# Kernel optimization log

Measured on AMD Instinct MI355X. Metric: run time of the kernel, lower is better.

The kernel has to match this reference:

```python
import jax, jax.numpy as jnp
import numpy as np

# Config (matches init_kwargs): channels=64, num_ell=16 (lmax=3), correlation=3,
# num_elements=10, output irreps L=0 (dim 1) and L=1 (dim 3), n_nodes=2048.
N, C, I, E = 2048, 64, 16, 10
K3, K2, K1 = 4, 2, 1  # number of coupling paths per correlation order
DIMS = (1, 3)         # output irrep dims (0e, 1o)


def setup_inputs() -> dict:
    key = jax.random.key(0)
    ks = jax.random.split(key, 24)
    inp = {}
    inp['node_feats'] = jax.random.normal(ks[0], (N, C, I), dtype=jnp.float32)
    inp['sc'] = jax.random.normal(ks[1], (N, sum(C * d for d in DIMS)), dtype=jnp.float32)
    idx = jax.random.randint(ks[2], (N,), 0, E)
    inp['node_attrs'] = jax.nn.one_hot(idx, E, dtype=jnp.float32)
    # Clebsch-Gordan-structured basis tensors (random placeholders, correct shapes)
    for t, d in enumerate(DIMS):
        inp[f'U3_{t}'] = 0.1 * jax.random.normal(ks[3 + 6 * t], (d, I, I, I, K3), dtype=jnp.float32)
        inp[f'U2_{t}'] = 0.1 * jax.random.normal(ks[4 + 6 * t], (d, I, I, K2), dtype=jnp.float32)
        inp[f'U1_{t}'] = 0.1 * jax.random.normal(ks[5 + 6 * t], (d, I, K1), dtype=jnp.float32)
        inp[f'W3_{t}'] = jax.random.normal(ks[6 + 6 * t], (E, K3, C), dtype=jnp.float32) / np.sqrt(K3)
        inp[f'W2_{t}'] = jax.random.normal(ks[7 + 6 * t], (E, K2, C), dtype=jnp.float32) / np.sqrt(K2)
        inp[f'W1_{t}'] = jax.random.normal(ks[8 + 6 * t], (E, K1, C), dtype=jnp.float32)
        inp[f'Wlin_{t}'] = jax.random.normal(ks[15 + t], (C, C), dtype=jnp.float32)
    return inp


def _contract_irrep(x, y, U3, U2, U1, W3, W2, W1):
    # MACE Contraction: highest correlation first, then fold in x one order at a time.
    out = jnp.einsum('mijlk,ekc,bcl,be->bcmij', U3, W3, x, y)   # [N,C,d,I,I]
    c2 = jnp.einsum('mijk,ekc,be->bcmij', U2, W2, y) + out
    out = jnp.einsum('bcmij,bcj->bcmi', c2, x)                   # [N,C,d,I]
    c1 = jnp.einsum('mik,ekc,be->bcmi', U1, W1, y) + out
    return jnp.einsum('bcmi,bci->bcm', c1, x)                    # [N,C,d]


def reference(node_feats, sc, node_attrs,
              U3_0, U2_0, U1_0, W3_0, W2_0, W1_0, Wlin_0,
              U3_1, U2_1, U1_1, W3_1, W2_1, W1_1, Wlin_1):
    x, y = node_feats, node_attrs
    f0 = _contract_irrep(x, y, U3_0, U2_0, U1_0, W3_0, W2_0, W1_0)  # [N,C,1]
    f1 = _contract_irrep(x, y, U3_1, U2_1, U1_1, W3_1, W2_1, W1_1)  # [N,C,3]
    inv_sqrt_c = 1.0 / np.sqrt(C).astype(np.float32)
    l0 = jnp.einsum('bcd,cf->bfd', f0, Wlin_0) * inv_sqrt_c
    l1 = jnp.einsum('bcd,cf->bfd', f1, Wlin_1) * inv_sqrt_c
    out = jnp.concatenate([l0.reshape(l0.shape[0], -1), l1.reshape(l1.shape[0], -1)], axis=1)
    return out + sc
```

## Files before the change

### kernel.cpp

```cpp
#include <hip/hip_runtime.h>

#define NND   2048
#define NC    64
#define NI    16
#define NE    10
#define NT3   816
#define NT2   136
#define NPAD  1024
#define CHUNK 32
#define MAXIT 74
#define M2ST  36

#define OFF_U3S   0u
#define OFF_U2S   52224u
#define OFF_TBL2  56576u
#define OFF_PTBL  60672u
#define OFF_NLIST 61248u
#define OFF_BST   69440u
#define OFF_ITEMS 69504u
#define OFF_NIT   69824u
#define OFF_F     69888u

__device__ inline void unrank3(int p, int& i, int& j, int& l) {
  int rem = p, i_ = 0;
  for (;;) { int cnt = (16 - i_) * (17 - i_) / 2; if (rem < cnt) break; rem -= cnt; ++i_; }
  int j_ = i_;
  for (;;) { int cnt = 16 - j_; if (rem < cnt) break; rem -= cnt; ++j_; }
  i = i_; j = j_; l = j_ + rem;
}
__device__ inline void unrank2(int q, int& i, int& j) {
  int rem = q, i_ = 0;
  for (;;) { int cnt = 16 - i_; if (rem < cnt) break; rem -= cnt; ++i_; }
  i = i_; j = i_ + rem;
}
__device__ inline int rank2(int a, int b) { return a * 16 - (a * (a - 1)) / 2 + (b - a); }

__device__ inline float4 u3read(const float* U3, int m, int a, int b, int d) {
  return *(const float4*)(U3 + (size_t)((((m * 16 + a) * 16 + b) * 16 + d) * 4));
}
__device__ inline float4 f4mul(float4 a, float4 b) {
  return make_float4(a.x * b.x, a.y * b.y, a.z * b.z, a.w * b.w);
}

__global__ __launch_bounds__(256) void k_prep(
    const float* __restrict__ U3_0, const float* __restrict__ U3_1,
    const float* __restrict__ U2_0, const float* __restrict__ U2_1,
    const float* __restrict__ y,
    float* __restrict__ U3sym, float* __restrict__ U2sym,
    int* __restrict__ tbl2, int* __restrict__ ptbl, int* __restrict__ nlist,
    int* __restrict__ bstart, int* __restrict__ items, int* __restrict__ nitems) {
  int tid = threadIdx.x;
  int bid = blockIdx.x;
  if (bid == 0) {
    for (int p = tid; p < NPAD; p += 256) {
      int a, qq;
      if (p < NT3) {
        int i, j, l; unrank3(p, i, j, l);
        a = l; qq = rank2(i, j);
      } else if (p < NT3 + NT2) {
        a = 16; qq = p - NT3;
      } else if (p < NT3 + NT2 + 16) {
        a = 16; qq = 136 + (p - NT3 - NT2);
      } else {
        a = 16; qq = 152;
      }
      tbl2[p] = a | (qq << 8);
    }
    for (int q = tid; q < NT2; q += 256) {
      int i, j; unrank2(q, i, j);
      ptbl[q] = i | (j << 8);
    }
    for (int idx = tid; idx < 4 * NT2; idx += 256) {
      int m4 = idx / NT2, q = idx - m4 * NT2;
      const float* U2 = (m4 == 0) ? U2_0 : U2_1;
      int mloc = (m4 == 0) ? 0 : (m4 - 1);
      int i, j; unrank2(q, i, j);
      const float* ua = U2 + (size_t)(((mloc * 16 + i) * 16 + j) * 2);
      float s0 = ua[0], s1 = ua[1];
      if (i != j) {
        const float* ub = U2 + (size_t)(((mloc * 16 + j) * 16 + i) * 2);
        s0 += ub[0]; s1 += ub[1];
      }
      float* o = U2sym + (size_t)(m4 * NT2 + q) * 2;
      o[0] = s0; o[1] = s1;
    }
  } else if (bid == 1) {
    __shared__ int cnt[NE], cur[NE];
    if (tid < NE) cnt[tid] = 0;
    __syncthreads();
    int mye[NND / 256];
    for (int rr = 0; rr < NND / 256; ++rr) {
      int b = tid + rr * 256;
      int e = 0;
      for (int ee = 0; ee < NE; ++ee)
        if (y[b * NE + ee] > 0.5f) e = ee;
      mye[rr] = e;
      atomicAdd(&cnt[e], 1);
    }
    __syncthreads();
    if (tid == 0) {
      int run = 0, ni = 0;
      for (int e = 0; e < NE; ++e) {
        bstart[e] = run; cur[e] = run;
        int nchunks = (cnt[e] + CHUNK - 1) / CHUNK;
        for (int ch = 0; ch < nchunks; ++ch) items[ni++] = e | (ch << 4);
        run += cnt[e];
      }
      bstart[NE] = run;
      nitems[0] = ni;
    }
    __syncthreads();
    for (int rr = 0; rr < NND / 256; ++rr) {
      int b = tid + rr * 256;
      int pos = atomicAdd(&cur[mye[rr]], 1);
      nlist[pos] = b;
    }
  } else {
    int idx = (bid - 2) * 256 + tid;
    if (idx < 4 * NT3) {
      int m4 = idx / NT3, tau = idx - m4 * NT3;
      const float* U3 = (m4 == 0) ? U3_0 : U3_1;
      int mloc = (m4 == 0) ? 0 : (m4 - 1);
      int i, j, l; unrank3(tau, i, j, l);
      float4 s = u3read(U3, mloc, i, j, l);
      if (i == j && j == l) {
      } else if (i == j) {
        float4 b1 = u3read(U3, mloc, i, l, i), b2 = u3read(U3, mloc, l, i, i);
        s.x += b1.x + b2.x; s.y += b1.y + b2.y; s.z += b1.z + b2.z; s.w += b1.w + b2.w;
      } else if (j == l) {
        float4 b1 = u3read(U3, mloc, j, i, j), b2 = u3read(U3, mloc, j, j, i);
        s.x += b1.x + b2.x; s.y += b1.y + b2.y; s.z += b1.z + b2.z; s.w += b1.w + b2.w;
      } else {
        float4 b1 = u3read(U3, mloc, i, l, j), b2 = u3read(U3, mloc, j, i, l);
        float4 b3 = u3read(U3, mloc, j, l, i), b4 = u3read(U3, mloc, l, i, j);
        float4 b5 = u3read(U3, mloc, l, j, i);
        s.x += b1.x + b2.x + b3.x + b4.x + b5.x;
        s.y += b1.y + b2.y + b3.y + b4.y + b5.y;
        s.z += b1.z + b2.z + b3.z + b4.z + b5.z;
        s.w += b1.w + b2.w + b3.w + b4.w + b5.w;
      }
      ((float4*)U3sym)[m4 * NT3 + tau] = s;
    }
  }
}

__device__ inline float4 mergef4(float4 x, float4 y, int m, int lane) {
  float4 r;
  bool hi = (lane & m) != 0;
  { float t = x.x + __shfl_xor(x.x, m); float u = y.x + __shfl_xor(y.x, m); r.x = hi ? u : t; }
  { float t = x.y + __shfl_xor(x.y, m); float u = y.y + __shfl_xor(y.y, m); r.y = hi ? u : t; }
  { float t = x.z + __shfl_xor(x.z, m); float u = y.z + __shfl_xor(y.z, m); r.z = hi ? u : t; }
  { float t = x.w + __shfl_xor(x.w, m); float u = y.w + __shfl_xor(y.w, m); r.w = hi ? u : t; }
  return r;
}

__global__ __launch_bounds__(256) void k_main(
    const float* __restrict__ x,
    const float* __restrict__ U3sym, const float* __restrict__ U2sym,
    const float* __restrict__ U1_0, const float* __restrict__ U1_1,
    const float* __restrict__ W3_0, const float* __restrict__ W3_1,
    const float* __restrict__ W2_0, const float* __restrict__ W2_1,
    const float* __restrict__ W1_0, const float* __restrict__ W1_1,
    const int* __restrict__ tbl2, const int* __restrict__ ptbl,
    const int* __restrict__ nlist, const int* __restrict__ bstart,
    const int* __restrict__ items, const int* __restrict__ nitems,
    float* __restrict__ f) {
  int bx = blockIdx.x;
  if (bx >= nitems[0]) return;
  __shared__ __align__(16) float4 sS4[NPAD];
  __shared__ __align__(16) float  sM2[153 * M2ST];
  __shared__ __align__(16) float  sxT[17 * M2ST];
  int tid = threadIdx.x;
  int w = tid >> 6, lane = tid & 63;
  int item = items[bx];
  int e = item & 15, ch = item >> 4;
  int c = blockIdx.y;
  int bs = bstart[e], be = bstart[e + 1];
  int base = bs + ch * CHUNK;
  int n_here = be - base; if (n_here > CHUNK) n_here = CHUNK;

  int t2r[16];
#pragma unroll
  for (int q = 0; q < 16; ++q) t2r[q] = tbl2[lane + (q << 6)];

  float w30[4], w31[4], w20[2], w21[2];
#pragma unroll
  for (int k = 0; k < 4; ++k) {
    w30[k] = W3_0[e * 256 + k * 64 + c];
    w31[k] = W3_1[e * 256 + k * 64 + c];
  }
#pragma unroll
  for (int k = 0; k < 2; ++k) {
    w20[k] = W2_0[e * 128 + k * 64 + c];
    w21[k] = W2_1[e * 128 + k * 64 + c];
  }
  float w10 = W1_0[e * 64 + c], w11 = W1_1[e * 64 + c];

  const float4* U3s4 = (const float4*)U3sym;
  float4 sreg[4];
#pragma unroll
  for (int k = 0; k < 4; ++k) {
    int p = tid + (k << 8);
    float4 o = make_float4(0.f, 0.f, 0.f, 0.f);
    if (p < NT3) {
      float4 u0 = U3s4[p];
      float4 u1 = U3s4[NT3 + p];
      float4 u2 = U3s4[2 * NT3 + p];
      float4 u3 = U3s4[3 * NT3 + p];
      o.x = u0.x * w30[0] + u0.y * w30[1] + u0.z * w30[2] + u0.w * w30[3];
      o.y = u1.x * w31[0] + u1.y * w31[1] + u1.z * w31[2] + u1.w * w31[3];
      o.z = u2.x * w31[0] + u2.y * w31[1] + u2.z * w31[2] + u2.w * w31[3];
      o.w = u3.x * w31[0] + u3.y * w31[1] + u3.z * w31[2] + u3.w * w31[3];
    } else if (p < NT3 + NT2) {
      int q = p - NT3;
      const float* u0 = U2sym + (size_t)(0 * NT2 + q) * 2;
      const float* u1 = U2sym + (size_t)(1 * NT2 + q) * 2;
      const float* u2 = U2sym + (size_t)(2 * NT2 + q) * 2;
      const float* u3 = U2sym + (size_t)(3 * NT2 + q) * 2;
      o.x = u0[0] * w20[0] + u0[1] * w20[1];
      o.y = u1[0] * w21[0] + u1[1] * w21[1];
      o.z = u2[0] * w21[0] + u2[1] * w21[1];
      o.w = u3[0] * w21[0] + u3[1] * w21[1];
    } else if (p < NT3 + NT2 + 16) {
      int i = p - NT3 - NT2;
      o.x = U1_0[i] * w10;
      o.y = U1_1[i] * w11;
      o.z = U1_1[16 + i] * w11;
      o.w = U1_1[32 + i] * w11;
    }
    sS4[p] = o;
    sreg[k] = o;
  }
  for (int rr = 0; rr < 2; ++rr) {
    int r = (tid >> 4) + 16 * rr, i = tid & 15;
    float v = 0.f;
    if (r < n_here) {
      int b = nlist[base + r];
      v = x[(size_t)b * (NC * NI) + c * NI + i];
    }
    sxT[i * M2ST + r] = v;
  }
  if (tid < CHUNK) sxT[16 * M2ST + tid] = 1.0f;
  __syncthreads();
  for (int idx = tid; idx < 153 * 8; idx += 256) {
    int qq = idx >> 3, rq = (idx & 7) << 2;
    float4 v;
    if (qq < NT2) {
      int pv = ptbl[qq];
      float4 xi = *(const float4*)&sxT[(pv & 255) * M2ST + rq];
      float4 xj = *(const float4*)&sxT[(pv >> 8) * M2ST + rq];
      v = f4mul(xi, xj);
    } else if (qq < 152) {
      v = *(const float4*)&sxT[(qq - 136) * M2ST + rq];
    } else {
      v = make_float4(0.f, 0.f, 0.f, 0.f);
    }
    *(float4*)&sM2[qq * M2ST + rq] = v;
  }
  __syncthreads();

  float4 acc[8];
#pragma unroll
  for (int t = 0; t < 8; ++t) acc[t] = make_float4(0.f, 0.f, 0.f, 0.f);
  int rbase = 8 * w;
#pragma unroll
  for (int q = 0; q < 16; ++q) {
    int t2 = t2r[q];
    int ai = t2 & 255, qq = t2 >> 8;
    float4 xa = *(const float4*)&sxT[ai * M2ST + rbase];
    float4 xb = *(const float4*)&sxT[ai * M2ST + rbase + 4];
    float4 ma = *(const float4*)&sM2[qq * M2ST + rbase];
    float4 mb = *(const float4*)&sM2[qq * M2ST + rbase + 4];
    float4 sv;
    if ((q & 3) == w) sv = sreg[q >> 2];
    else              sv = sS4[lane + (q << 6)];
    float mo[8];
    mo[0] = xa.x * ma.x; mo[1] = xa.y * ma.y; mo[2] = xa.z * ma.z; mo[3] = xa.w * ma.w;
    mo[4] = xb.x * mb.x; mo[5] = xb.y * mb.y; mo[6] = xb.z * mb.z; mo[7] = xb.w * mb.w;
#pragma unroll
    for (int t = 0; t < 8; ++t) {
      acc[t].x = fmaf(sv.x, mo[t], acc[t].x);
      acc[t].y = fmaf(sv.y, mo[t], acc[t].y);
      acc[t].z = fmaf(sv.z, mo[t], acc[t].z);
      acc[t].w = fmaf(sv.w, mo[t], acc[t].w);
    }
  }
  float4 s01 = mergef4(acc[0], acc[1], 32, lane);
  float4 s23 = mergef4(acc[2], acc[3], 32, lane);
  float4 s45 = mergef4(acc[4], acc[5], 32, lane);
  float4 s67 = mergef4(acc[6], acc[7], 32, lane);
  float4 t0 = mergef4(s01, s23, 16, lane);
  float4 t1 = mergef4(s45, s67, 16, lane);
  float4 u = mergef4(t0, t1, 8, lane);
#pragma unroll
  for (int m = 4; m >= 1; m >>= 1) {
    u.x += __shfl_xor(u.x, m);
    u.y += __shfl_xor(u.y, m);
    u.z += __shfl_xor(u.z, m);
    u.w += __shfl_xor(u.w, m);
  }
  if ((lane & 7) == 0) {
    int k = ((lane >> 5) & 1) | (((lane >> 4) & 1) << 1) | (((lane >> 3) & 1) << 2);
    int r = rbase + k;
    if (r < n_here) {
      float4* fo = (float4*)f;
      fo[(size_t)nlist[base + r] * 64 + c] = u;
    }
  }
}

__global__ __launch_bounds__(256) void k_out(
    const float* __restrict__ f, const float* __restrict__ Wl0,
    const float* __restrict__ Wl1, const float* __restrict__ sc,
    float* __restrict__ out) {
  __shared__ float sW0[4096], sW1[4096], sf[4][256];
  int tid = threadIdx.x;
  for (int u = tid; u < 4096; u += 256) { sW0[u] = Wl0[u]; sW1[u] = Wl1[u]; }
  int nb = blockIdx.x * 4;
  for (int u = tid; u < 1024; u += 256) {
    int r = u >> 8, k = u & 255;
    sf[r][k] = f[(size_t)(nb + r) * 256 + k];
  }
  __syncthreads();
  int o = tid;
  int fch, msel; const float* Wl;
  if (o < 64) { fch = o; msel = 0; Wl = sW0; }
  else { int j = o - 64; fch = j / 3; msel = 1 + (j % 3); Wl = sW1; }
#pragma unroll
  for (int r = 0; r < 4; ++r) {
    float acc = 0.f;
#pragma unroll 8
    for (int cc = 0; cc < 64; ++cc)
      acc = fmaf(sf[r][cc * 4 + msel], Wl[cc * 64 + fch], acc);
    int b = nb + r;
    out[(size_t)b * 256 + o] = 0.125f * acc + sc[(size_t)b * 256 + o];
  }
}

extern "C" void kernel_launch(void* const* d_in, const int* in_sizes, int n_in,
                              void* d_out, int out_size, void* d_ws, size_t ws_size,
                              hipStream_t stream) {
  const float* node_feats = (const float*)d_in[0];
  const float* sc   = (const float*)d_in[1];
  const float* y    = (const float*)d_in[2];
  const float* U3_0 = (const float*)d_in[3];
  const float* U2_0 = (const float*)d_in[4];
  const float* U1_0 = (const float*)d_in[5];
  const float* W3_0 = (const float*)d_in[6];
  const float* W2_0 = (const float*)d_in[7];
  const float* W1_0 = (const float*)d_in[8];
  const float* Wl_0 = (const float*)d_in[9];
  const float* U3_1 = (const float*)d_in[10];
  const float* U2_1 = (const float*)d_in[11];
  const float* U1_1 = (const float*)d_in[12];
  const float* W3_1 = (const float*)d_in[13];
  const float* W2_1 = (const float*)d_in[14];
  const float* W1_1 = (const float*)d_in[15];
  const float* Wl_1 = (const float*)d_in[16];
  float* out = (float*)d_out;
  char* ws = (char*)d_ws;

  float* U3sym = (float*)(ws + OFF_U3S);
  float* U2sym = (float*)(ws + OFF_U2S);
  int*   tbl2  = (int*)(ws + OFF_TBL2);
  int*   ptbl  = (int*)(ws + OFF_PTBL);
  int*   nlist = (int*)(ws + OFF_NLIST);
  int*   bst   = (int*)(ws + OFF_BST);
  int*   items = (int*)(ws + OFF_ITEMS);
  int*   nit   = (int*)(ws + OFF_NIT);
  float* f     = (float*)(ws + OFF_F);

  k_prep<<<15, 256, 0, stream>>>(U3_0, U3_1, U2_0, U2_1, y,
                                 U3sym, U2sym, tbl2, ptbl, nlist, bst, items, nit);
  k_main<<<dim3(MAXIT, NC), 256, 0, stream>>>(node_feats, U3sym, U2sym,
                                              U1_0, U1_1, W3_0, W3_1, W2_0, W2_1,
                                              W1_0, W1_1, tbl2, ptbl, nlist, bst,
                                              items, nit, f);
  k_out<<<NND / 4, 256, 0, stream>>>(f, Wl_0, Wl_1, sc, out);
}
```

Before: 188.7 us.

## Precompute per-element/channel S tables and halve node chunk size

Adds a k_buildS kernel that computes the weighted symmetric coupling table S once per (element, channel) into workspace, so k_main loads it instead of recomputing it from U3sym/U2sym and the weights in every block. It also halves CHUNK to 16 nodes per block, roughly doubling the grid, shrinking per-thread accumulators and adding an occupancy hint of 5 blocks. The trade-off is an extra kernel launch, a ~10 MB workspace write and read, and more blocks that each reload S. Without enough workspace it falls back to the old in-kernel computation.

Measured after the change: 345.6 us. +83.1%, slower.

```diff
diff --git a/kernel.cpp b/kernel.cpp
--- a/kernel.cpp
+++ b/kernel.cpp
@@ -7,9 +7,9 @@
 #define NT3   816
 #define NT2   136
 #define NPAD  1024
-#define CHUNK 32
-#define MAXIT 74
-#define M2ST  36
+#define CHUNK 16
+#define MAXIT 138
+#define M2ST  20
 
 #define OFF_U3S   0u
 #define OFF_U2S   52224u
@@ -18,8 +18,10 @@
 #define OFF_NLIST 61248u
 #define OFF_BST   69440u
 #define OFF_ITEMS 69504u
-#define OFF_NIT   69824u
-#define OFF_F     69888u
+#define OFF_NIT   70144u
+#define OFF_F     70208u
+#define OFF_S     2167360u
+#define WS_NEED   12653120u
 
 __device__ inline void unrank3(int p, int& i, int& j, int& l) {
   int rem = p, i_ = 0;
@@ -144,45 +146,14 @@
   }
 }
 
-__device__ inline float4 mergef4(float4 x, float4 y, int m, int lane) {
-  float4 r;
-  bool hi = (lane & m) != 0;
-  { float t = x.x + __shfl_xor(x.x, m); float u = y.x + __shfl_xor(y.x, m); r.x = hi ? u : t; }
-  { float t = x.y + __shfl_xor(x.y, m); float u = y.y + __shfl_xor(y.y, m); r.y = hi ? u : t; }
-  { float t = x.z + __shfl_xor(x.z, m); float u = y.z + __shfl_xor(y.z, m); r.z = hi ? u : t; }
-  { float t = x.w + __shfl_xor(x.w, m); float u = y.w + __shfl_xor(y.w, m); r.w = hi ? u : t; }
-  return r;
-}
-
-__global__ __launch_bounds__(256) void k_main(
-    const float* __restrict__ x,
+__global__ __launch_bounds__(256) void k_buildS(
     const float* __restrict__ U3sym, const float* __restrict__ U2sym,
     const float* __restrict__ U1_0, const float* __restrict__ U1_1,
     const float* __restrict__ W3_0, const float* __restrict__ W3_1,
     const float* __restrict__ W2_0, const float* __restrict__ W2_1,
     const float* __restrict__ W1_0, const float* __restrict__ W1_1,
-    const int* __restrict__ tbl2, const int* __restrict__ ptbl,
-    const int* __restrict__ nlist, const int* __restrict__ bstart,
-    const int* __restrict__ items, const int* __restrict__ nitems,
-    float* __restrict__ f) {
-  int bx = blockIdx.x;
-  if (bx >= nitems[0]) return;
-  __shared__ __align__(16) float4 sS4[NPAD];
-  __shared__ __align__(16) float  sM2[153 * M2ST];
-  __shared__ __align__(16) float  sxT[17 * M2ST];
-  int tid = threadIdx.x;
-  int w = tid >> 6, lane = tid & 63;
-  int item = items[bx];
-  int e = item & 15, ch = item >> 4;
-  int c = blockIdx.y;
-  int bs = bstart[e], be = bstart[e + 1];
-  int base = bs + ch * CHUNK;
-  int n_here = be - base; if (n_here > CHUNK) n_here = CHUNK;
-
-  int t2r[16];
-#pragma unroll
-  for (int q = 0; q < 16; ++q) t2r[q] = tbl2[lane + (q << 6)];
-
+    float* __restrict__ S) {
+  int e = blockIdx.x, c = blockIdx.y, tid = threadIdx.x;
   float w30[4], w31[4], w20[2], w21[2];
 #pragma unroll
   for (int k = 0; k < 4; ++k) {
@@ -195,9 +166,8 @@
     w21[k] = W2_1[e * 128 + k * 64 + c];
   }
   float w10 = W1_0[e * 64 + c], w11 = W1_1[e * 64 + c];
-
   const float4* U3s4 = (const float4*)U3sym;
-  float4 sreg[4];
+  float4* Sg = (float4*)S + (size_t)(e * 64 + c) * NPAD;
 #pragma unroll
   for (int k = 0; k < 4; ++k) {
     int p = tid + (k << 8);
@@ -228,22 +198,120 @@
       o.z = U1_1[16 + i] * w11;
       o.w = U1_1[32 + i] * w11;
     }
-    sS4[p] = o;
-    sreg[k] = o;
-  }
-  for (int rr = 0; rr < 2; ++rr) {
-    int r = (tid >> 4) + 16 * rr, i = tid & 15;
+    Sg[p] = o;
+  }
+}
+
+__device__ inline float4 mergef4(float4 x, float4 y, int m, int lane) {
+  float4 r;
+  bool hi = (lane & m) != 0;
+  { float t = x.x + __shfl_xor(x.x, m); float u = y.x + __shfl_xor(y.x, m); r.x = hi ? u : t; }
+  { float t = x.y + __shfl_xor(x.y, m); float u = y.y + __shfl_xor(y.y, m); r.y = hi ? u : t; }
+  { float t = x.z + __shfl_xor(x.z, m); float u = y.z + __shfl_xor(y.z, m); r.z = hi ? u : t; }
+  { float t = x.w + __shfl_xor(x.w, m); float u = y.w + __shfl_xor(y.w, m); r.w = hi ? u : t; }
+  return r;
+}
+
+__global__ __launch_bounds__(256, 5) void k_main(
+    const float* __restrict__ x, const float* __restrict__ Sglob, int useS,
+    const float* __restrict__ U3sym, const float* __restrict__ U2sym,
+    const float* __restrict__ U1_0, const float* __restrict__ U1_1,
+    const float* __restrict__ W3_0, const float* __restrict__ W3_1,
+    const float* __restrict__ W2_0, const float* __restrict__ W2_1,
+    const float* __restrict__ W1_0, const float* __restrict__ W1_1,
+    const int* __restrict__ tbl2, const int* __restrict__ ptbl,
+    const int* __restrict__ nlist, const int* __restrict__ bstart,
+    const int* __restrict__ items, const int* __restrict__ nitems,
+    float* __restrict__ f) {
+  int bx = blockIdx.x;
+  if (bx >= nitems[0]) return;
+  __shared__ __align__(16) float4 sS4[NPAD];
+  __shared__ __align__(16) float  sM2[153 * M2ST];
+  __shared__ __align__(16) float  sxT[17 * M2ST];
+  int tid = threadIdx.x;
+  int w = tid >> 6, lane = tid & 63;
+  int item = items[bx];
+  int e = item & 15, ch = item >> 4;
+  int c = blockIdx.y;
+  int bs = bstart[e], be = bstart[e + 1];
+  int base = bs + ch * CHUNK;
+  int n_here = be - base; if (n_here > CHUNK) n_here = CHUNK;
+
+  int t2r[16];
+#pragma unroll
+  for (int q = 0; q < 16; ++q) t2r[q] = tbl2[lane + (q << 6)];
+
+  float4 sreg[4];
+  if (useS) {
+    const float4* Sg = (const float4*)Sglob + (size_t)(e * 64 + c) * NPAD;
+#pragma unroll
+    for (int k = 0; k < 4; ++k) {
+      int p = tid + (k << 8);
+      float4 o = Sg[p];
+      sS4[p] = o;
+      sreg[k] = o;
+    }
+  } else {
+    float w30[4], w31[4], w20[2], w21[2];
+#pragma unroll
+    for (int k = 0; k < 4; ++k) {
+      w30[k] = W3_0[e * 256 + k * 64 + c];
+      w31[k] = W3_1[e * 256 + k * 64 + c];
+    }
+#pragma unroll
+    for (int k = 0; k < 2; ++k) {
+      w20[k] = W2_0[e * 128 + k * 64 + c];
+      w21[k] = W2_1[e * 128 + k * 64 + c];
+    }
+    float w10 = W1_0[e * 64 + c], w11 = W1_1[e * 64 + c];
+    const float4* U3s4 = (const float4*)U3sym;
+#pragma unroll
+    for (int k = 0; k < 4; ++k) {
+      int p = tid + (k << 8);
+      float4 o = make_float4(0.f, 0.f, 0.f, 0.f);
+      if (p < NT3) {
+        float4 u0 = U3s4[p];
+        float4 u1 = U3s4[NT3 + p];
+        float4 u2 = U3s4[2 * NT3 + p];
+        float4 u3 = U3s4[3 * NT3 + p];
+        o.x = u0.x * w30[0] + u0.y * w30[1] + u0.z * w30[2] + u0.w * w30[3];
+        o.y = u1.x * w31[0] + u1.y * w31[1] + u1.z * w31[2] + u1.w * w31[3];
+        o.z = u2.x * w31[0] + u2.y * w31[1] + u2.z * w31[2] + u2.w * w31[3];
+        o.w = u3.x * w31[0] + u3.y * w31[1] + u3.z * w31[2] + u3.w * w31[3];
+      } else if (p < NT3 + NT2) {
+        int q = p - NT3;
+        const float* u0 = U2sym + (size_t)(0 * NT2 + q) * 2;
+        const float* u1 = U2sym + (size_t)(1 * NT2 + q) * 2;
+        const float* u2 = U2sym + (size_t)(2 * NT2 + q) * 2;
+        const float* u3 = U2sym + (size_t)(3 * NT2 + q) * 2;
+        o.x = u0[0] * w20[0] + u0[1] * w20[1];
+        o.y = u1[0] * w21[0] + u1[1] * w21[1];
+        o.z = u2[0] * w21[0] + u2[1] * w21[1];
+        o.w = u3[0] * w21[0] + u3[1] * w21[1];
+      } else if (p < NT3 + NT2 + 16) {
+        int i = p - NT3 - NT2;
+        o.x = U1_0[i] * w10;
+        o.y = U1_1[i] * w11;
+        o.z = U1_1[16 + i] * w11;
+        o.w = U1_1[32 + i] * w11;
+      }
+      sS4[p] = o;
+      sreg[k] = o;
+    }
+  }
+  {
+    int r = tid >> 4, i = tid & 15;
     float v = 0.f;
     if (r < n_here) {
       int b = nlist[base + r];
       v = x[(size_t)b * (NC * NI) + c * NI + i];
     }
     sxT[i * M2ST + r] = v;
-  }
-  if (tid < CHUNK) sxT[16 * M2ST + tid] = 1.0f;
+    if (tid < CHUNK) sxT[16 * M2ST + tid] = 1.0f;
+  }
   __syncthreads();
-  for (int idx = tid; idx < 153 * 8; idx += 256) {
-    int qq = idx >> 3, rq = (idx & 7) << 2;
+  for (int idx = tid; idx < 153 * 4; idx += 256) {
+    int qq = idx >> 2, rq = (idx & 3) << 2;
     float4 v;
     if (qq < NT2) {
       int pv = ptbl[qq];
@@ -259,26 +327,23 @@
   }
   __syncthreads();
 
-  float4 acc[8];
-#pragma unroll
-  for (int t = 0; t < 8; ++t) acc[t] = make_float4(0.f, 0.f, 0.f, 0.f);
-  int rbase = 8 * w;
+  float4 acc[4];
+#pragma unroll
+  for (int t = 0; t < 4; ++t) acc[t] = make_float4(0.f, 0.f, 0.f, 0.f);
+  int rbase = 4 * w;
 #pragma unroll
   for (int q = 0; q < 16; ++q) {
     int t2 = t2r[q];
     int ai = t2 & 255, qq = t2 >> 8;
     float4 xa = *(const float4*)&sxT[ai * M2ST + rbase];
-    float4 xb = *(const float4*)&sxT[ai * M2ST + rbase + 4];
     float4 ma = *(const float4*)&sM2[qq * M2ST + rbase];
-    float4 mb = *(const float4*)&sM2[qq * M2ST + rbase + 4];
     float4 sv;
     if ((q & 3) == w) sv = sreg[q >> 2];
     else              sv = sS4[lane + (q << 6)];
-    float mo[8];
+    float mo[4];
     mo[0] = xa.x * ma.x; mo[1] = xa.y * ma.y; mo[2] = xa.z * ma.z; mo[3] = xa.w * ma.w;
-    mo[4] = xb.x * mb.x; mo[5] = xb.y * mb.y; mo[6] = xb.z * mb.z; mo[7] = xb.w * mb.w;
-#pragma unroll
-    for (int t = 0; t < 8; ++t) {
+#pragma unroll
+    for (int t = 0; t < 4; ++t) {
       acc[t].x = fmaf(sv.x, mo[t], acc[t].x);
       acc[t].y = fmaf(sv.y, mo[t], acc[t].y);
       acc[t].z = fmaf(sv.z, mo[t], acc[t].z);
@@ -287,20 +352,16 @@
   }
   float4 s01 = mergef4(acc[0], acc[1], 32, lane);
   float4 s23 = mergef4(acc[2], acc[3], 32, lane);
-  float4 s45 = mergef4(acc[4], acc[5], 32, lane);
-  float4 s67 = mergef4(acc[6], acc[7], 32, lane);
-  float4 t0 = mergef4(s01, s23, 16, lane);
-  float4 t1 = mergef4(s45, s67, 16, lane);
-  float4 u = mergef4(t0, t1, 8, lane);
-#pragma unroll
-  for (int m = 4; m >= 1; m >>= 1) {
+  float4 u = mergef4(s01, s23, 16, lane);
+#pragma unroll
+  for (int m = 8; m >= 1; m >>= 1) {
     u.x += __shfl_xor(u.x, m);
     u.y += __shfl_xor(u.y, m);
     u.z += __shfl_xor(u.z, m);
     u.w += __shfl_xor(u.w, m);
   }
-  if ((lane & 7) == 0) {
-    int k = ((lane >> 5) & 1) | (((lane >> 4) & 1) << 1) | (((lane >> 3) & 1) << 2);
+  if ((lane & 15) == 0) {
+    int k = ((lane >> 5) & 1) | (((lane >> 4) & 1) << 1);
     int r = rbase + k;
     if (r < n_here) {
       float4* fo = (float4*)f;
@@ -369,10 +430,17 @@
   int*   items = (int*)(ws + OFF_ITEMS);
   int*   nit   = (int*)(ws + OFF_NIT);
   float* f     = (float*)(ws + OFF_F);
+  float* S     = (float*)(ws + OFF_S);
+  int useS = (ws_size >= (size_t)WS_NEED) ? 1 : 0;
 
   k_prep<<<15, 256, 0, stream>>>(U3_0, U3_1, U2_0, U2_1, y,
                                  U3sym, U2sym, tbl2, ptbl, nlist, bst, items, nit);
-  k_main<<<dim3(MAXIT, NC), 256, 0, stream>>>(node_feats, U3sym, U2sym,
+  if (useS) {
+    k_buildS<<<dim3(NE, NC), 256, 0, stream>>>(U3sym, U2sym, U1_0, U1_1,
+                                               W3_0, W3_1, W2_0, W2_1,
+                                               W1_0, W1_1, S);
+  }
+  k_main<<<dim3(MAXIT, NC), 256, 0, stream>>>(node_feats, S, useS, U3sym, U2sym,
                                               U1_0, U1_1, W3_0, W3_1, W2_0, W2_1,
                                               W1_0, W1_1, tbl2, ptbl, nlist, bst,
                                               items, nit, f);
```
